# Kernel optimization log

Hardware: AMD Instinct MI355X
Metric: run time of the kernel (lower is better)

## Reference

```python
import jax, jax.numpy as jnp
import numpy as np

D_MODEL = 512
NHEAD = 8
HEAD_DIM = D_MODEL // NHEAD
D_FF = 2048
EPS = 1e-5


def _linear_params(key, d_in, d_out):
    kw, kb = jax.random.split(key)
    bound = 1.0 / np.sqrt(d_in)
    W = jax.random.uniform(kw, (d_out, d_in), jnp.float32, -bound, bound)
    b = jax.random.uniform(kb, (d_out,), jnp.float32, -bound, bound)
    return W, b


def setup_inputs() -> dict:
    key = jax.random.key(0)
    ks = jax.random.split(key, 8)
    src = jax.random.normal(ks[0], (4, 2048, D_MODEL), jnp.float32)
    Wq, bq = _linear_params(ks[1], D_MODEL, D_MODEL)
    Wk, bk = _linear_params(ks[2], D_MODEL, D_MODEL)
    Wv, bv = _linear_params(ks[3], D_MODEL, D_MODEL)
    Wo, bo = _linear_params(ks[4], D_MODEL, D_MODEL)
    W1, b1 = _linear_params(ks[5], D_MODEL, D_FF)
    W2, b2 = _linear_params(ks[6], D_FF, D_MODEL)
    g1 = jnp.ones((D_MODEL,), jnp.float32)
    be1 = jnp.zeros((D_MODEL,), jnp.float32)
    g2 = jnp.ones((D_MODEL,), jnp.float32)
    be2 = jnp.zeros((D_MODEL,), jnp.float32)
    return dict(src=src, Wq=Wq, bq=bq, Wk=Wk, bk=bk, Wv=Wv, bv=bv,
                Wo=Wo, bo=bo, W1=W1, b1=b1, W2=W2, b2=b2,
                g1=g1, be1=be1, g2=g2, be2=be2)


def _layer_norm(x, g, b):
    mu = jnp.mean(x, axis=-1, keepdims=True)
    var = jnp.mean(jnp.square(x - mu), axis=-1, keepdims=True)
    return (x - mu) / jnp.sqrt(var + EPS) * g + b


def reference(src, Wq, bq, Wk, bk, Wv, bv, Wo, bo, W1, b1, W2, b2, g1, be1, g2, be2):
    B, T, D = src.shape
    scale = np.sqrt(HEAD_DIM).astype(np.float32)
    # Projections (torch Linear: x @ W.T + b)
    Q = (src @ Wq.T + bq).reshape(B, T, NHEAD, HEAD_DIM).transpose(0, 2, 1, 3)
    K = (src @ Wk.T + bk).reshape(B, T, NHEAD, HEAD_DIM).transpose(0, 2, 1, 3)
    V = (src @ Wv.T + bv).reshape(B, T, NHEAD, HEAD_DIM).transpose(0, 2, 1, 3)
    # Explicit QK^T -> softmax -> V (no mask, dropout=0)
    scores = jnp.einsum('bhqd,bhkd->bhqk', Q, K) / scale  # (B,H,T,T)
    attn = jax.nn.softmax(scores, axis=-1)
    ctx = jnp.einsum('bhqk,bhkd->bhqd', attn, V)
    ctx = ctx.transpose(0, 2, 1, 3).reshape(B, T, D)
    attn_out = ctx @ Wo.T + bo
    # Add & Norm 1
    x = _layer_norm(src + attn_out, g1, be1)
    # FFN: Linear -> GELU -> Linear
    h = jax.nn.gelu(x @ W1.T + b1, approximate=False)
    ffn_out = h @ W2.T + b2
    # Add & Norm 2
    return _layer_norm(x + ffn_out, g2, be2)
```

## Files before the change

kernel.cpp:

```cpp
#include <hip/hip_runtime.h>
#include <hip/hip_bf16.h>
#include <hip/hip_fp16.h>
#include <math.h>

typedef __bf16 bf16_t;
typedef __bf16 bf16x8 __attribute__((ext_vector_type(8)));
typedef __bf16 bf16x2 __attribute__((ext_vector_type(2)));
typedef float  f32x4  __attribute__((ext_vector_type(4)));

#define D_MODEL 512
#define NHEAD   8
#define HD      64
#define D_FF    2048
#define TOKENS  8192
#define SEQ     2048
#define BATCH   4

__device__ __forceinline__ void gload16(const bf16_t* g, bf16_t* l)
{
    __builtin_amdgcn_global_load_lds(
        (const __attribute__((address_space(1))) void*)g,
        (__attribute__((address_space(3))) void*)l,
        16, 0, 0);
}

__device__ __forceinline__ void cvt4(const float* s, bf16_t* d)
{
    float4 v = *(const float4*)s;
    alignas(8) bf16_t t[4] = {(bf16_t)v.x, (bf16_t)v.y, (bf16_t)v.z, (bf16_t)v.w};
    *(uint2*)d = *(const uint2*)t;
}

__device__ __forceinline__ void barrier_raw() { asm volatile("s_barrier" ::: "memory"); }
__device__ __forceinline__ void sched_fence() { __builtin_amdgcn_sched_barrier(0); }

__device__ __forceinline__ float gelu_f(float x)
{
    const float y = fabsf(x) * 0.70710678118654752f;
    const float t = 1.0f / fmaf(0.3275911f, y, 1.0f);
    float p = fmaf(1.061405429f, t, -1.453152027f);
    p = fmaf(p, t, 1.421413741f);
    p = fmaf(p, t, -0.284496736f);
    p = fmaf(p, t, 0.254829592f);
    p *= t;
    const float e = __builtin_amdgcn_exp2f(-y * y * 1.4426950408889634f);
    float erfv = 1.0f - p * e;
    erfv = (x < 0.f) ? -erfv : erfv;
    return 0.5f * x * (1.0f + erfv);
}

__global__ void cvt_weights(const float* __restrict__ src,
                            const float* __restrict__ Wq, const float* __restrict__ Wk,
                            const float* __restrict__ Wv, const float* __restrict__ Wo,
                            const float* __restrict__ W1, const float* __restrict__ W2,
                            const float* __restrict__ bq, const float* __restrict__ bk,
                            const float* __restrict__ bv,
                            bf16_t* __restrict__ Xb,
                            bf16_t* __restrict__ Wqkvb, bf16_t* __restrict__ Wob,
                            bf16_t* __restrict__ W1b, bf16_t* __restrict__ W2b,
                            float* __restrict__ bqkv, float* __restrict__ zbias)
{
    int i = blockIdx.x * 256 + threadIdx.x;
    if (i < 1048576) { cvt4(src + (size_t)i * 4, Xb + (size_t)i * 4); return; }
    i -= 1048576;
    if (i < 65536)        cvt4(Wq + (size_t)i * 4,            Wqkvb + (size_t)i * 4);
    else if (i < 131072)  cvt4(Wk + (size_t)(i - 65536) * 4,  Wqkvb + (size_t)i * 4);
    else if (i < 196608)  cvt4(Wv + (size_t)(i - 131072) * 4, Wqkvb + (size_t)i * 4);
    else if (i < 262144)  cvt4(Wo + (size_t)(i - 196608) * 4, Wob + (size_t)(i - 196608) * 4);
    else if (i < 524288)  cvt4(W1 + (size_t)(i - 262144) * 4, W1b + (size_t)(i - 262144) * 4);
    else if (i < 786432)  cvt4(W2 + (size_t)(i - 524288) * 4, W2b + (size_t)(i - 524288) * 4);
    else if (i < 786816) {
        int j = i - 786432;
        const float* s = (j < 128) ? bq + j * 4 : (j < 256) ? bk + (j - 128) * 4
                                                            : bv + (j - 256) * 4;
        *(float4*)(bqkv + (j & 127) * 4 + (j >> 7) * 512) = *(const float4*)s;
    } else if (i < 786944) {
        int j = i - 786816;
        *(float4*)(zbias + j * 4) = make_float4(0.f, 0.f, 0.f, 0.f);
    }
}

template <int BM, int EPI, bool SPLIT2>
__global__ __launch_bounds__(256)
void gemm_bt(const bf16_t* __restrict__ A, const bf16_t* __restrict__ B,
             const float* __restrict__ bias, const float* __restrict__ biasz,
             void* __restrict__ Cout, bf16_t* __restrict__ vt,
             int M, int N, int K)
{
    constexpr int MI = BM / 32;
    constexpr int NA = BM / 32;
    __shared__ bf16_t sA[2][BM][64];
    __shared__ bf16_t sB[2][128][64];
    bf16_t* sAf = &sA[0][0][0];
    bf16_t* sBf = &sB[0][0][0];

    const int tid  = threadIdx.x;
    const int wave = tid >> 6;
    const int lane = tid & 63;
    const int g    = lane >> 4;
    const int c16  = lane & 15;
    const int wm   = (wave >> 1) * (BM / 2);
    const int wn   = (wave & 1) * 64;
    const int m0   = blockIdx.y * BM;
    const int n0   = blockIdx.x * 128;

    const int zz    = SPLIT2 ? blockIdx.z : 0;
    const int Keff  = SPLIT2 ? (K >> 1) : K;
    const int kbase = zz * Keff;
    const float* bptr = (SPLIT2 && zz) ? biasz : bias;

    const f32x4 fz = {0.f, 0.f, 0.f, 0.f};
    f32x4 acc[MI][4];
#pragma unroll
    for (int i = 0; i < MI; i++)
#pragma unroll
        for (int j = 0; j < 4; j++) acc[i][j] = fz;

    const bf16_t* gA[NA]; int fa[NA];
#pragma unroll
    for (int i = 0; i < NA; i++) {
        const int f = i * 256 + tid, row = f >> 3, l = (f & 7) ^ (row & 7);
        fa[i] = f;
        gA[i] = A + (size_t)(m0 + row) * K + kbase + l * 8;
    }
    const bf16_t* gB[4]; int fb[4];
#pragma unroll
    for (int i = 0; i < 4; i++) {
        const int f = i * 256 + tid, row = f >> 3, l = (f & 7) ^ (row & 7);
        fb[i] = f;
        gB[i] = B + (size_t)(n0 + row) * K + kbase + l * 8;
    }

    auto stage = [&](int ko, int buf) {
        bf16_t* dA = sAf + buf * (BM * 64);
        bf16_t* dB = sBf + buf * 8192;
#pragma unroll
        for (int i = 0; i < NA; i++) gload16(gA[i] + ko, dA + fa[i] * 8);
#pragma unroll
        for (int i = 0; i < 4; i++)  gload16(gB[i] + ko, dB + fb[i] * 8);
    };

    stage(0, 0);
    stage(64, 1);

    const int NS = Keff >> 6;
    for (int s = 0; s < NS; ++s) {
        const int cur = s & 1;
        if (s + 1 < NS) {
            if constexpr (NA == 2) asm volatile("s_waitcnt vmcnt(6)" ::: "memory");
            else                   asm volatile("s_waitcnt vmcnt(8)" ::: "memory");
        } else {
            asm volatile("s_waitcnt vmcnt(0)" ::: "memory");
        }
        barrier_raw();
        sched_fence();

#pragma unroll
        for (int sub = 0; sub < 2; ++sub) {
            const int ck = (((sub * 4 + g) ^ (c16 & 7))) * 8;
            bf16x8 af[MI], bfr[4];
#pragma unroll
            for (int i = 0; i < MI; i++)
                af[i] = *(const bf16x8*)&sA[cur][wm + i * 16 + c16][ck];
#pragma unroll
            for (int j = 0; j < 4; j++)
                bfr[j] = *(const bf16x8*)&sB[cur][wn + j * 16 + c16][ck];
#pragma unroll
            for (int mi = 0; mi < MI; mi++)
#pragma unroll
                for (int ni = 0; ni < 4; ni++)
                    acc[mi][ni] = __builtin_amdgcn_mfma_f32_16x16x32_bf16(
                        af[mi], bfr[ni], acc[mi][ni], 0, 0, 0);
        }

        sched_fence();
        barrier_raw();
        if (s + 2 < NS) stage((s + 2) << 6, cur);
        sched_fence();
    }

    __half* outh = (__half*)Cout + (size_t)zz * M * N;
#pragma unroll
    for (int mi = 0; mi < MI; mi++) {
#pragma unroll
        for (int ni = 0; ni < 4; ni++) {
            const int col = n0 + wn + ni * 16 + c16;
            const float bv = bptr[col];
#pragma unroll
            for (int r = 0; r < 4; r++) {
                const int row = m0 + wm + mi * 16 + g * 4 + r;
                float v = acc[mi][ni][r] + bv;
                if (EPI == 1) v = gelu_f(v);
                if (EPI == 2) {
                    outh[(size_t)row * N + col] = (__half)v;
                } else if (EPI == 3 && col >= 1024) {
                    const int c1 = col - 1024;
                    const int h = c1 >> 6, d = c1 & 63;
                    const int b = row >> 11;
                    const int ts = row & 2047;
                    const int tile = ts >> 6, w = ts & 63;
                    const int p = (w & 0x23)
                                | ((w & 0x08) << 1)
                                | ((w & 0x04) << 1)
                                | ((w & 0x10) >> 2);
                    vt[((size_t)((b * 8 + h) * 64 + d)) * SEQ + tile * 64 + p] =
                        (bf16_t)v;
                } else {
                    ((bf16_t*)Cout)[(size_t)row * N + col] = (bf16_t)v;
                }
            }
        }
    }
}

__global__ __launch_bounds__(512)
__attribute__((amdgpu_waves_per_eu(6)))
void flash_attn(const bf16_t* __restrict__ qkv, const bf16_t* __restrict__ vt,
                bf16_t* __restrict__ ctx)
{
    __shared__ bf16_t sK[3][64][64];
    __shared__ bf16_t sVt[3][64][64];

    const int bh = blockIdx.y;
    const int b = bh >> 3, h = bh & 7;
    const int q0 = blockIdx.x * 128;
    const int tid = threadIdx.x;
    const int wave = tid >> 6, lane = tid & 63;
    const int g = lane >> 4, c16 = lane & 15;

    const float qscale = 0.125f * 1.4426950408889634f;
    bf16x8 aq[2];
#pragma unroll
    for (int ks = 0; ks < 2; ks++) {
        bf16x8 v = *(const bf16x8*)(qkv +
            ((size_t)(b * SEQ + q0 + wave * 16 + c16)) * 1536 +
            h * 64 + ks * 32 + g * 8);
#pragma unroll
        for (int j = 0; j < 8; j++) v[j] = (bf16_t)((float)v[j] * qscale);
        aq[ks] = v;
    }

    const f32x4 fz = {0.f, 0.f, 0.f, 0.f};
    f32x4 acc_oT[4];
#pragma unroll
    for (int dt = 0; dt < 4; dt++) acc_oT[dt] = fz;
    float l_acc = 0.f;

    const int f0 = tid, r0 = f0 >> 3, l0 = (f0 & 7) ^ (r0 & 7);
    const bf16_t* gK0 = qkv + ((size_t)(b * SEQ + r0)) * 1536 + 512 + h * 64 + l0 * 8;
    const bf16_t* gV0 = vt + ((size_t)(bh * 64 + r0)) * SEQ + l0 * 8;
    bf16_t* lK = &sK[0][0][0];
    bf16_t* lV = &sVt[0][0][0];

    auto stageKV = [&](int t) {
        const int bo = (t % 3) * 4096;
        const size_t kv = (size_t)t * 64;
        gload16(gK0 + kv * 1536, lK + bo + f0 * 8);
        gload16(gV0 + kv,        lV + bo + f0 * 8);
    };

    f32x4 accs[4];
    auto qk_mfma = [&](int cur) {
#pragma unroll
        for (int tt = 0; tt < 4; tt++) accs[tt] = fz;
#pragma unroll
        for (int ks = 0; ks < 2; ks++) {
            const int pc = ((ks * 4 + g) ^ (c16 & 7)) * 8;
#pragma unroll
            for (int tt = 0; tt < 4; tt++) {
                bf16x8 ak = *(const bf16x8*)&sK[cur][tt * 16 + c16][pc];
                accs[tt] = __builtin_amdgcn_mfma_f32_16x16x32_bf16(ak, aq[ks], accs[tt], 0, 0, 0);
            }
        }
    };

    bf16x8 pb[2];
    auto pv_mfma = [&](int cur) {
#pragma unroll
        for (int kv = 0; kv < 2; kv++) {
            const int pc = ((kv * 4 + g) ^ (c16 & 7)) * 8;
#pragma unroll
            for (int dt = 0; dt < 4; dt++) {
                bf16x8 av = *(const bf16x8*)&sVt[cur][dt * 16 + c16][pc];
                acc_oT[dt] = __builtin_amdgcn_mfma_f32_16x16x32_bf16(av, pb[kv], acc_oT[dt], 0, 0, 0);
            }
        }
    };

    auto softmax_pack = [&]() {
#pragma unroll
        for (int tt = 0; tt < 4; tt++) {
            float s = 0.f;
#pragma unroll
            for (int r = 0; r < 4; r++) {
                float p = __builtin_amdgcn_exp2f(accs[tt][r]);
                accs[tt][r] = p;
                s += p;
            }
            l_acc += s;
        }
#pragma unroll
        for (int kv = 0; kv < 2; kv++)
#pragma unroll
            for (int j = 0; j < 8; j++)
                pb[kv][j] = (bf16_t)accs[kv * 2 + (j >> 2)][j & 3];
    };

    stageKV(0);
    stageKV(1);

    for (int it = 0; it < 32; ++it) {
        const int cur = it % 3;
        if (it < 31) asm volatile("s_waitcnt vmcnt(2)" ::: "memory");
        else         asm volatile("s_waitcnt vmcnt(0)" ::: "memory");
        barrier_raw();

        __builtin_amdgcn_s_setprio(1);
        qk_mfma(cur);
        __builtin_amdgcn_s_setprio(0);
        softmax_pack();
        __builtin_amdgcn_s_setprio(1);
        pv_mfma(cur);
        __builtin_amdgcn_s_setprio(0);

        if (it + 2 < 32) stageKV(it + 2);
    }

    {
        float l = l_acc;
        l += __shfl_xor(l, 16);
        l += __shfl_xor(l, 32);
        const float inv = 1.0f / l;
        const int token = q0 + wave * 16 + c16;
        bf16_t* dst = ctx + ((size_t)(b * SEQ + token)) * 512 + h * 64 + g * 4;
#pragma unroll
        for (int dt = 0; dt < 4; dt++) {
            alignas(8) bf16_t o4[4];
#pragma unroll
            for (int r = 0; r < 4; r++) o4[r] = (bf16_t)(acc_oT[dt][r] * inv);
            *(uint2*)(dst + dt * 16) = *(const uint2*)o4;
        }
    }
}

__global__ __launch_bounds__(256)
void add_ln3(const float* __restrict__ a, const __half* __restrict__ b,
             const __half* __restrict__ c,
             const float* __restrict__ gamma, const float* __restrict__ beta,
             float* __restrict__ outf, bf16_t* __restrict__ outb)
{
    const int row  = blockIdx.x * 4 + (threadIdx.x >> 6);
    const int lane = threadIdx.x & 63;
    const size_t base = (size_t)row * 512 + lane * 8;

    int4 braw = *(const int4*)(b + base);
    int4 craw = *(const int4*)(c + base);
    const __half* bh = (const __half*)&braw;
    const __half* ch = (const __half*)&craw;

    float v[8];
#pragma unroll
    for (int hh = 0; hh < 2; hh++) {
        float4 av = *(const float4*)(a + base + hh * 4);
        v[hh * 4 + 0] = av.x + (float)bh[hh * 4 + 0] + (float)ch[hh * 4 + 0];
        v[hh * 4 + 1] = av.y + (float)bh[hh * 4 + 1] + (float)ch[hh * 4 + 1];
        v[hh * 4 + 2] = av.z + (float)bh[hh * 4 + 2] + (float)ch[hh * 4 + 2];
        v[hh * 4 + 3] = av.w + (float)bh[hh * 4 + 3] + (float)ch[hh * 4 + 3];
    }

    float s = 0.f;
#pragma unroll
    for (int i = 0; i < 8; i++) s += v[i];
#pragma unroll
    for (int off = 32; off > 0; off >>= 1) s += __shfl_xor(s, off);
    const float mu = s * (1.f / 512.f);

    float q = 0.f;
#pragma unroll
    for (int i = 0; i < 8; i++) { float d = v[i] - mu; q += d * d; }
#pragma unroll
    for (int off = 32; off > 0; off >>= 1) q += __shfl_xor(q, off);
    const float rstd = rsqrtf(q * (1.f / 512.f) + 1e-5f);

    float4 g0 = *(const float4*)(gamma + lane * 8);
    float4 g1 = *(const float4*)(gamma + lane * 8 + 4);
    float4 e0 = *(const float4*)(beta + lane * 8);
    float4 e1 = *(const float4*)(beta + lane * 8 + 4);
    const float gg[8] = {g0.x, g0.y, g0.z, g0.w, g1.x, g1.y, g1.z, g1.w};
    const float ee[8] = {e0.x, e0.y, e0.z, e0.w, e1.x, e1.y, e1.z, e1.w};

    float o[8];
#pragma unroll
    for (int i = 0; i < 8; i++) o[i] = (v[i] - mu) * rstd * gg[i] + ee[i];

    *(float4*)(outf + base)     = make_float4(o[0], o[1], o[2], o[3]);
    *(float4*)(outf + base + 4) = make_float4(o[4], o[5], o[6], o[7]);
    if (outb) {
        alignas(16) bf16_t ob[8];
#pragma unroll
        for (int i = 0; i < 8; i++) ob[i] = (bf16_t)o[i];
        *(int4*)(outb + base) = *(const int4*)ob;
    }
}

extern "C" void kernel_launch(void* const* d_in, const int* in_sizes, int n_in,
                              void* d_out, int out_size, void* d_ws, size_t ws_size,
                              hipStream_t stream)
{
    const float* src = (const float*)d_in[0];
    const float* Wq  = (const float*)d_in[1];  const float* bq  = (const float*)d_in[2];
    const float* Wk  = (const float*)d_in[3];  const float* bk  = (const float*)d_in[4];
    const float* Wv  = (const float*)d_in[5];  const float* bv  = (const float*)d_in[6];
    const float* Wo  = (const float*)d_in[7];  const float* bo  = (const float*)d_in[8];
    const float* W1  = (const float*)d_in[9];  const float* b1  = (const float*)d_in[10];
    const float* W2  = (const float*)d_in[11]; const float* b2  = (const float*)d_in[12];
    const float* g1  = (const float*)d_in[13]; const float* be1 = (const float*)d_in[14];
    const float* g2  = (const float*)d_in[15]; const float* be2 = (const float*)d_in[16];
    float* out = (float*)d_out;

    char* ws = (char*)d_ws;
    size_t off = 0;
    auto alloc = [&](size_t bytes) -> void* {
        void* p = ws + off;
        off = (off + bytes + 255) & ~(size_t)255;
        return p;
    };

    bf16_t* Xb    = (bf16_t*)alloc((size_t)TOKENS * 512 * 2);
    bf16_t* Wqkvb = (bf16_t*)alloc((size_t)1536 * 512 * 2);
    bf16_t* Wob   = (bf16_t*)alloc((size_t)512 * 512 * 2);
    bf16_t* W1b   = (bf16_t*)alloc((size_t)2048 * 512 * 2);
    bf16_t* W2b   = (bf16_t*)alloc((size_t)512 * 2048 * 2);
    float*  bqkv  = (float*)alloc(1536 * 4);
    float*  zbias = (float*)alloc(512 * 4);
    bf16_t* QKV   = (bf16_t*)alloc((size_t)TOKENS * 1536 * 2);
    bf16_t* Vt    = (bf16_t*)alloc((size_t)32 * 64 * SEQ * 2);
    bf16_t* CTX   = (bf16_t*)alloc((size_t)TOKENS * 512 * 2);
    __half* ATTa  = (__half*)alloc((size_t)TOKENS * 512 * 2);
    __half* ATTb  = (__half*)alloc((size_t)TOKENS * 512 * 2);
    float*  X1    = (float*)alloc((size_t)TOKENS * 512 * 4);
    bf16_t* X1b   = (bf16_t*)alloc((size_t)TOKENS * 512 * 2);

    bf16_t* H    = QKV;
    __half* FFNa = ATTa;
    __half* FFNb = ATTb;

    cvt_weights<<<7170, 256, 0, stream>>>(src, Wq, Wk, Wv, Wo, W1, W2, bq, bk, bv,
                                          Xb, Wqkvb, Wob, W1b, W2b, bqkv, zbias);

    gemm_bt<128, 3, false><<<dim3(12, 64), 256, 0, stream>>>(
        Xb, Wqkvb, bqkv, zbias, QKV, Vt, TOKENS, 1536, 512);

    flash_attn<<<dim3(16, 32), 512, 0, stream>>>(QKV, Vt, CTX);

    gemm_bt<64, 2, true><<<dim3(4, 128, 2), 256, 0, stream>>>(
        CTX, Wob, bo, zbias, ATTa, nullptr, TOKENS, 512, 512);

    add_ln3<<<2048, 256, 0, stream>>>(src, ATTa, ATTb, g1, be1, X1, X1b);

    gemm_bt<128, 1, false><<<dim3(16, 64), 256, 0, stream>>>(
        X1b, W1b, b1, zbias, H, nullptr, TOKENS, 2048, 512);

    gemm_bt<64, 2, true><<<dim3(4, 128, 2), 256, 0, stream>>>(
        H, W2b, b2, zbias, FFNa, nullptr, TOKENS, 512, 2048);

    add_ln3<<<2048, 256, 0, stream>>>(X1, FFNa, FFNb, g2, be2, out, nullptr);
}
```

Before: 282.8 us.

## Give each attention wave two query tiles with half the waves per block

The flash attention kernel now runs 4 waves per block instead of 8, and each wave handles 32 query rows (two 16-row tiles) instead of 16. Each K/V fragment read from LDS is reused for two MFMAs, halving LDS read traffic per unit of math. Each thread now issues two async loads per stage, and the vmcnt wait is adjusted to match. The cost is doubled accumulator and P registers, a lower waves-per-EU target, and fewer waves available to hide latency.

```diff
diff --git a/kernel.cpp b/kernel.cpp
--- a/kernel.cpp
+++ b/kernel.cpp
@@ -213,8 +213,8 @@
     }
 }
 
-__global__ __launch_bounds__(512)
-__attribute__((amdgpu_waves_per_eu(6)))
+__global__ __launch_bounds__(256)
+__attribute__((amdgpu_waves_per_eu(3)))
 void flash_attn(const bf16_t* __restrict__ qkv, const bf16_t* __restrict__ vt,
                 bf16_t* __restrict__ ctx)
 {
@@ -229,26 +229,33 @@
     const int g = lane >> 4, c16 = lane & 15;
 
     const float qscale = 0.125f * 1.4426950408889634f;
-    bf16x8 aq[2];
-#pragma unroll
-    for (int ks = 0; ks < 2; ks++) {
-        bf16x8 v = *(const bf16x8*)(qkv +
-            ((size_t)(b * SEQ + q0 + wave * 16 + c16)) * 1536 +
-            h * 64 + ks * 32 + g * 8);
-#pragma unroll
-        for (int j = 0; j < 8; j++) v[j] = (bf16_t)((float)v[j] * qscale);
-        aq[ks] = v;
-    }
+    bf16x8 aq[2][2];
+#pragma unroll
+    for (int qt = 0; qt < 2; qt++)
+#pragma unroll
+        for (int ks = 0; ks < 2; ks++) {
+            bf16x8 v = *(const bf16x8*)(qkv +
+                ((size_t)(b * SEQ + q0 + wave * 32 + qt * 16 + c16)) * 1536 +
+                h * 64 + ks * 32 + g * 8);
+#pragma unroll
+            for (int j = 0; j < 8; j++) v[j] = (bf16_t)((float)v[j] * qscale);
+            aq[qt][ks] = v;
+        }
 
     const f32x4 fz = {0.f, 0.f, 0.f, 0.f};
-    f32x4 acc_oT[4];
-#pragma unroll
-    for (int dt = 0; dt < 4; dt++) acc_oT[dt] = fz;
-    float l_acc = 0.f;
-
-    const int f0 = tid, r0 = f0 >> 3, l0 = (f0 & 7) ^ (r0 & 7);
+    f32x4 acc_oT[4][2];
+#pragma unroll
+    for (int dt = 0; dt < 4; dt++)
+#pragma unroll
+        for (int qt = 0; qt < 2; qt++) acc_oT[dt][qt] = fz;
+    float l_acc[2] = {0.f, 0.f};
+
+    const int f0 = tid,        r0 = f0 >> 3, l0 = (f0 & 7) ^ (r0 & 7);
+    const int f1 = tid + 256,  r1 = f1 >> 3, l1 = (f1 & 7) ^ (r1 & 7);
     const bf16_t* gK0 = qkv + ((size_t)(b * SEQ + r0)) * 1536 + 512 + h * 64 + l0 * 8;
+    const bf16_t* gK1 = qkv + ((size_t)(b * SEQ + r1)) * 1536 + 512 + h * 64 + l1 * 8;
     const bf16_t* gV0 = vt + ((size_t)(bh * 64 + r0)) * SEQ + l0 * 8;
+    const bf16_t* gV1 = vt + ((size_t)(bh * 64 + r1)) * SEQ + l1 * 8;
     bf16_t* lK = &sK[0][0][0];
     bf16_t* lV = &sVt[0][0][0];
 
@@ -256,25 +263,30 @@
         const int bo = (t % 3) * 4096;
         const size_t kv = (size_t)t * 64;
         gload16(gK0 + kv * 1536, lK + bo + f0 * 8);
+        gload16(gK1 + kv * 1536, lK + bo + f1 * 8);
         gload16(gV0 + kv,        lV + bo + f0 * 8);
-    };
-
-    f32x4 accs[4];
+        gload16(gV1 + kv,        lV + bo + f1 * 8);
+    };
+
+    f32x4 accs[4][2];
     auto qk_mfma = [&](int cur) {
 #pragma unroll
-        for (int tt = 0; tt < 4; tt++) accs[tt] = fz;
+        for (int tt = 0; tt < 4; tt++)
+#pragma unroll
+            for (int qt = 0; qt < 2; qt++) accs[tt][qt] = fz;
 #pragma unroll
         for (int ks = 0; ks < 2; ks++) {
             const int pc = ((ks * 4 + g) ^ (c16 & 7)) * 8;
 #pragma unroll
             for (int tt = 0; tt < 4; tt++) {
                 bf16x8 ak = *(const bf16x8*)&sK[cur][tt * 16 + c16][pc];
-                accs[tt] = __builtin_amdgcn_mfma_f32_16x16x32_bf16(ak, aq[ks], accs[tt], 0, 0, 0);
+                accs[tt][0] = __builtin_amdgcn_mfma_f32_16x16x32_bf16(ak, aq[0][ks], accs[tt][0], 0, 0, 0);
+                accs[tt][1] = __builtin_amdgcn_mfma_f32_16x16x32_bf16(ak, aq[1][ks], accs[tt][1], 0, 0, 0);
             }
         }
     };
 
-    bf16x8 pb[2];
+    bf16x8 pb[2][2];
     auto pv_mfma = [&](int cur) {
 #pragma unroll
         for (int kv = 0; kv < 2; kv++) {
@@ -282,28 +294,33 @@
 #pragma unroll
             for (int dt = 0; dt < 4; dt++) {
                 bf16x8 av = *(const bf16x8*)&sVt[cur][dt * 16 + c16][pc];
-                acc_oT[dt] = __builtin_amdgcn_mfma_f32_16x16x32_bf16(av, pb[kv], acc_oT[dt], 0, 0, 0);
+                acc_oT[dt][0] = __builtin_amdgcn_mfma_f32_16x16x32_bf16(av, pb[0][kv], acc_oT[dt][0], 0, 0, 0);
+                acc_oT[dt][1] = __builtin_amdgcn_mfma_f32_16x16x32_bf16(av, pb[1][kv], acc_oT[dt][1], 0, 0, 0);
             }
         }
     };
 
     auto softmax_pack = [&]() {
 #pragma unroll
-        for (int tt = 0; tt < 4; tt++) {
-            float s = 0.f;
-#pragma unroll
-            for (int r = 0; r < 4; r++) {
-                float p = __builtin_amdgcn_exp2f(accs[tt][r]);
-                accs[tt][r] = p;
-                s += p;
+        for (int tt = 0; tt < 4; tt++)
+#pragma unroll
+            for (int qt = 0; qt < 2; qt++) {
+                float s = 0.f;
+#pragma unroll
+                for (int r = 0; r < 4; r++) {
+                    float p = __builtin_amdgcn_exp2f(accs[tt][qt][r]);
+                    accs[tt][qt][r] = p;
+                    s += p;
+                }
+                l_acc[qt] += s;
             }
-            l_acc += s;
-        }
-#pragma unroll
-        for (int kv = 0; kv < 2; kv++)
-#pragma unroll
-            for (int j = 0; j < 8; j++)
-                pb[kv][j] = (bf16_t)accs[kv * 2 + (j >> 2)][j & 3];
+#pragma unroll
+        for (int qt = 0; qt < 2; qt++)
+#pragma unroll
+            for (int kv = 0; kv < 2; kv++)
+#pragma unroll
+                for (int j = 0; j < 8; j++)
+                    pb[qt][kv][j] = (bf16_t)accs[kv * 2 + (j >> 2)][qt][j & 3];
     };
 
     stageKV(0);
@@ -311,7 +328,7 @@
 
     for (int it = 0; it < 32; ++it) {
         const int cur = it % 3;
-        if (it < 31) asm volatile("s_waitcnt vmcnt(2)" ::: "memory");
+        if (it < 31) asm volatile("s_waitcnt vmcnt(4)" ::: "memory");
         else         asm volatile("s_waitcnt vmcnt(0)" ::: "memory");
         barrier_raw();
 
@@ -326,18 +343,19 @@
         if (it + 2 < 32) stageKV(it + 2);
     }
 
-    {
-        float l = l_acc;
+#pragma unroll
+    for (int qt = 0; qt < 2; qt++) {
+        float l = l_acc[qt];
         l += __shfl_xor(l, 16);
         l += __shfl_xor(l, 32);
         const float inv = 1.0f / l;
-        const int token = q0 + wave * 16 + c16;
+        const int token = q0 + wave * 32 + qt * 16 + c16;
         bf16_t* dst = ctx + ((size_t)(b * SEQ + token)) * 512 + h * 64 + g * 4;
 #pragma unroll
         for (int dt = 0; dt < 4; dt++) {
             alignas(8) bf16_t o4[4];
 #pragma unroll
-            for (int r = 0; r < 4; r++) o4[r] = (bf16_t)(acc_oT[dt][r] * inv);
+            for (int r = 0; r < 4; r++) o4[r] = (bf16_t)(acc_oT[dt][qt][r] * inv);
             *(uint2*)(dst + dt * 16) = *(const uint2*)o4;
         }
     }
@@ -451,7 +469,7 @@
     gemm_bt<128, 3, false><<<dim3(12, 64), 256, 0, stream>>>(
         Xb, Wqkvb, bqkv, zbias, QKV, Vt, TOKENS, 1536, 512);
 
-    flash_attn<<<dim3(16, 32), 512, 0, stream>>>(QKV, Vt, CTX);
+    flash_attn<<<dim3(16, 32), 256, 0, stream>>>(QKV, Vt, CTX);
 
     gemm_bt<64, 2, true><<<dim3(4, 128, 2), 256, 0, stream>>>(
         CTX, Wob, bo, zbias, ATTa, nullptr, TOKENS, 512, 512);
```

New measurement: 283.9 us. About the same (+0.4%).
